# Kernel tuning notes

Hardware: AMD Instinct MI355X
Metric: run time of the kernel (lower is better)

## Reference

```python
import jax, jax.numpy as jnp
import numpy as np

NUM_TOKENS = 8192
D_MODEL = 512
D_FF = 1024
NUM_EXPERTS = 8
TOP_K = 2


def setup_inputs() -> dict:
    key = jax.random.key(0)
    k_x, k_r, k_w1, k_w2 = jax.random.split(key, 4)
    x = jax.random.normal(k_x, (NUM_TOKENS, D_MODEL), dtype=jnp.float32)
    # Router weight [num_experts, d_model]
    w_router = jax.random.normal(k_r, (NUM_EXPERTS, D_MODEL), dtype=jnp.float32) * 0.02
    # Expert weights stored as [E, N, K] (kernel convention: y = x @ W.T)
    w1 = jax.random.normal(k_w1, (NUM_EXPERTS, D_FF, D_MODEL), dtype=jnp.float32) * 0.02
    w2 = jax.random.normal(k_w2, (NUM_EXPERTS, D_MODEL, D_FF), dtype=jnp.float32) * 0.02
    return {"x": x, "w_router": w_router, "w1": w1, "w2": w2}


def reference(x, w_router, w1, w2):
    # Router: softmax over experts, top-k selection, renormalized gates
    logits = jnp.einsum("td,ed->te", x, w_router)            # [T, E]
    probs = jax.nn.softmax(logits, axis=-1)
    top_vals, top_idx = jax.lax.top_k(probs, TOP_K)           # [T, k]
    top_vals = top_vals / jnp.sum(top_vals, axis=-1, keepdims=True)

    # Combine weights per (token, expert): topk weight if selected else 0.
    # out[t] = sum_e gate[t,e] * W2[e] @ silu(W1[e] @ x[t])
    out = jnp.zeros_like(x)
    for e in range(NUM_EXPERTS):
        gate_e = jnp.sum(jnp.where(top_idx == e, top_vals, 0.0), axis=-1)  # [T]
        h = jax.nn.silu(jnp.einsum("td,fd->tf", x, w1[e]))                 # [T, d_ff]
        y = jnp.einsum("tf,df->td", h, w2[e])                              # [T, d]
        out = out + gate_e[:, None] * y
    return out
```

## Files before the change

### kernel.cpp

```cpp
#include <hip/hip_runtime.h>
#include <hip/hip_bf16.h>

#define NT 8192
#define DM 512
#define DF 1024
#define NE 8
#define MAXROWS (NT*2)

typedef __bf16 bf16_8 __attribute__((ext_vector_type(8)));
typedef float  f32_4  __attribute__((ext_vector_type(4)));
typedef unsigned short us8 __attribute__((ext_vector_type(8)));

__device__ inline unsigned short f2bf(float f) {
    unsigned int u = __float_as_uint(f);
    u = u + 0x7fffu + ((u >> 16) & 1u);
    return (unsigned short)(u >> 16);
}

__device__ inline bf16_8 as_bf(us8 v) { return __builtin_bit_cast(bf16_8, v); }

__device__ inline void gld16(const unsigned short* g, unsigned short* l) {
    __builtin_amdgcn_global_load_lds(
        (const __attribute__((address_space(1))) unsigned int*)g,
        (__attribute__((address_space(3))) unsigned int*)l, 16, 0, 0);
}

__global__ __launch_bounds__(256) void cast_kernel(const float* __restrict__ in,
                                                   unsigned short* __restrict__ out,
                                                   int n4) {
    int i = blockIdx.x * 256 + threadIdx.x;
    if (i >= n4) return;
    float4 v = ((const float4*)in)[i];
    ushort4 o;
    o.x = f2bf(v.x); o.y = f2bf(v.y); o.z = f2bf(v.z); o.w = f2bf(v.w);
    ((ushort4*)out)[i] = o;
}

__global__ __launch_bounds__(256) void router_kernel(const float* __restrict__ x,
                                                     const float* __restrict__ wr,
                                                     int* __restrict__ eidx,
                                                     float2* __restrict__ gates) {
    const int wid = threadIdx.x >> 6;
    const int lane = threadIdx.x & 63;
    const int t = blockIdx.x * 4 + wid;

    const float4* xrow = (const float4*)(x + (size_t)t * DM);
    float4 xv0 = xrow[lane * 2];
    float4 xv1 = xrow[lane * 2 + 1];

    float logit[NE];
#pragma unroll
    for (int e = 0; e < NE; ++e) {
        const float4* wrow = (const float4*)(wr + (size_t)e * DM);
        float4 w0 = wrow[lane * 2];
        float4 w1v = wrow[lane * 2 + 1];
        float s = xv0.x * w0.x + xv0.y * w0.y + xv0.z * w0.z + xv0.w * w0.w
                + xv1.x * w1v.x + xv1.y * w1v.y + xv1.z * w1v.z + xv1.w * w1v.w;
#pragma unroll
        for (int off = 32; off >= 1; off >>= 1) s += __shfl_xor(s, off);
        logit[e] = s;
    }

    if (lane == 0) {
        int i0 = 0; float m0 = logit[0];
#pragma unroll
        for (int e = 1; e < NE; ++e) if (logit[e] > m0) { m0 = logit[e]; i0 = e; }
        int i1 = -1; float m1 = -1e30f;
#pragma unroll
        for (int e = 0; e < NE; ++e) if (e != i0 && logit[e] > m1) { m1 = logit[e]; i1 = e; }
        float d = expf(m1 - m0);
        float g0 = 1.0f / (1.0f + d);
        float g1 = 1.0f - g0;
        eidx[t] = i0 | (i1 << 8);
        gates[t] = make_float2(g0, g1);
    }
}

__global__ __launch_bounds__(256) void build_lists_kernel(const int* __restrict__ eidx,
                                                          const float2* __restrict__ gates,
                                                          int* __restrict__ counts,
                                                          int* __restrict__ token_list,
                                                          float* __restrict__ gate_list) {
    const int e = blockIdx.x;
    const int tid = threadIdx.x;
    const int wid = tid >> 6, lane = tid & 63;
    __shared__ int wsum[4];
    __shared__ int base;
    if (tid == 0) base = 0;
    __syncthreads();
    for (int c = 0; c < NT; c += 256) {
        int t = c + tid;
        int ei = eidx[t];
        int i0 = ei & 0xff, i1 = (ei >> 8) & 0xff;
        bool match0 = (i0 == e), match1 = (i1 == e);
        bool m = match0 || match1;
        unsigned long long mask = __ballot(m);
        if (lane == 0) wsum[wid] = __popcll(mask);
        __syncthreads();
        int pre = 0;
#pragma unroll
        for (int w = 0; w < 4; ++w) if (w < wid) pre += wsum[w];
        int tot = wsum[0] + wsum[1] + wsum[2] + wsum[3];
        if (m) {
            int pos = base + pre + __popcll(mask & ((1ULL << lane) - 1ULL));
            token_list[e * NT + pos] = t;
            float2 g = gates[t];
            gate_list[e * NT + pos] = match0 ? g.x : g.y;
        }
        __syncthreads();
        if (tid == 0) base += tot;
        __syncthreads();
    }
    if (tid == 0) counts[e] = base;
}

__global__ void scan_kernel(const int* __restrict__ counts, int* __restrict__ offsets) {
    if (threadIdx.x == 0) {
        int s = 0;
        for (int e = 0; e < NE; ++e) { offsets[e] = s; s += counts[e]; }
    }
}

template <bool G1>
__global__ __launch_bounds__(256, 2) void moe_gemm(const unsigned short* __restrict__ Abase,
                                                   const unsigned short* __restrict__ Wbase,
                                                   unsigned short* __restrict__ h_out,
                                                   float* __restrict__ out,
                                                   const int* __restrict__ counts,
                                                   const int* __restrict__ offsets,
                                                   const int* __restrict__ token_list,
                                                   const float* __restrict__ gate_list) {
    constexpr int K = G1 ? DM : DF;
    constexpr int NCOLS = G1 ? DF : DM;
    constexpr int NSTEP = K / 64;
    constexpr int TILE_E = 128 * 64;
    const int e = blockIdx.z;
    const int cnt = counts[e];
    const int row0 = blockIdx.y * 128;
    if (row0 >= cnt) return;
    const int col0 = blockIdx.x * 128;
    const int off_e = offsets[e];

    __shared__ __align__(16) unsigned short Alds[2 * TILE_E];
    __shared__ __align__(16) unsigned short Blds[2 * TILE_E];

    const int tid = threadIdx.x;
    const int wid = tid >> 6;
    const int lane = tid & 63;

    const int g_oct = (lane & 7) ^ (lane >> 3);
    const unsigned short* gA[4];
    const unsigned short* gB[4];
    int ldsOff[4];
#pragma unroll
    for (int j = 0; j < 4; ++j) {
        int row_j = wid * 32 + j * 8 + (lane >> 3);
        int rr = min(row0 + row_j, cnt - 1);
        if (G1) {
            gA[j] = Abase + (size_t)token_list[e * NT + rr] * K + g_oct * 8;
        } else {
            gA[j] = Abase + (size_t)(off_e + rr) * K + g_oct * 8;
        }
        gB[j] = Wbase + ((size_t)e * NCOLS + col0 + row_j) * K + g_oct * 8;
        ldsOff[j] = (wid * 256 + j * 64) * 8;
    }

    const int wr = wid >> 1, wc = wid & 1;
    const int lrow = lane & 15;
    const int kc = lane >> 4;

    f32_4 acc[4][4];
#pragma unroll
    for (int m = 0; m < 4; ++m)
#pragma unroll
        for (int n = 0; n < 4; ++n) acc[m][n] = (f32_4){0.f, 0.f, 0.f, 0.f};

    auto issue = [&](int t) {
        int bb = t & 1;
        unsigned short* A_l = Alds + bb * TILE_E;
        unsigned short* B_l = Blds + bb * TILE_E;
        int k0 = t * 64;
#pragma unroll
        for (int j = 0; j < 4; ++j) {
            gld16(gA[j] + k0, A_l + ldsOff[j]);
            gld16(gB[j] + k0, B_l + ldsOff[j]);
        }
    };

    issue(0);
    for (int t = 0; t < NSTEP; ++t) {
        if (t + 1 < NSTEP) {
            issue(t + 1);
            asm volatile("s_waitcnt vmcnt(8)" ::: "memory");
        } else {
            asm volatile("s_waitcnt vmcnt(0)" ::: "memory");
        }
        __builtin_amdgcn_sched_barrier(0);
        __builtin_amdgcn_s_barrier();

        const unsigned short* A_l = Alds + (t & 1) * TILE_E;
        const unsigned short* B_l = Blds + (t & 1) * TILE_E;
#pragma unroll
        for (int s = 0; s < 2; ++s) {
            bf16_8 a[4], b[4];
#pragma unroll
            for (int m = 0; m < 4; ++m) {
                int row = wr * 64 + m * 16 + lrow;
                int oct = (s * 4 + kc) ^ (lrow & 7);
                a[m] = as_bf(*(const us8*)(A_l + row * 64 + oct * 8));
            }
#pragma unroll
            for (int n = 0; n < 4; ++n) {
                int row = wc * 64 + n * 16 + lrow;
                int oct = (s * 4 + kc) ^ (lrow & 7);
                b[n] = as_bf(*(const us8*)(B_l + row * 64 + oct * 8));
            }
#pragma unroll
            for (int m = 0; m < 4; ++m)
#pragma unroll
                for (int n = 0; n < 4; ++n)
                    acc[m][n] = __builtin_amdgcn_mfma_f32_16x16x32_bf16(a[m], b[n], acc[m][n], 0, 0, 0);
        }

        asm volatile("s_waitcnt lgkmcnt(0)" ::: "memory");
        __builtin_amdgcn_sched_barrier(0);
        __builtin_amdgcn_s_barrier();
    }

#pragma unroll
    for (int m = 0; m < 4; ++m) {
#pragma unroll
        for (int n = 0; n < 4; ++n) {
#pragma unroll
            for (int q = 0; q < 4; ++q) {
                int lr = wr * 64 + m * 16 + (lane >> 4) * 4 + q;
                int lc = wc * 64 + n * 16 + (lane & 15);
                int r = row0 + lr;
                if (r < cnt) {
                    float v = acc[m][n][q];
                    if (G1) {
                        v = v / (1.0f + expf(-v));
                        h_out[(size_t)(off_e + r) * DF + col0 + lc] = f2bf(v);
                    } else {
                        float g = gate_list[e * NT + r];
                        int tok = token_list[e * NT + r];
                        atomicAdd(&out[(size_t)tok * DM + col0 + lc], g * v);
                    }
                }
            }
        }
    }
}

extern "C" void kernel_launch(void* const* d_in, const int* in_sizes, int n_in,
                              void* d_out, int out_size, void* d_ws, size_t ws_size,
                              hipStream_t stream) {
    const float* x   = (const float*)d_in[0];
    const float* wrt = (const float*)d_in[1];
    const float* w1  = (const float*)d_in[2];
    const float* w2  = (const float*)d_in[3];
    float* out = (float*)d_out;

    char* ws = (char*)d_ws;
    size_t o = 0;
    auto alloc = [&](size_t bytes) { size_t r = o; o += (bytes + 255) & ~255UL; return r; };
    unsigned short* x_bf  = (unsigned short*)(ws + alloc((size_t)NT * DM * 2));
    unsigned short* w1_bf = (unsigned short*)(ws + alloc((size_t)NE * DF * DM * 2));
    unsigned short* w2_bf = (unsigned short*)(ws + alloc((size_t)NE * DM * DF * 2));
    unsigned short* h_bf  = (unsigned short*)(ws + alloc((size_t)MAXROWS * DF * 2));
    int*   counts     = (int*)(ws + alloc(NE * 4));
    int*   offsets    = (int*)(ws + alloc(NE * 4));
    int*   token_list = (int*)(ws + alloc((size_t)NE * NT * 4));
    float* gate_list  = (float*)(ws + alloc((size_t)NE * NT * 4));
    int*   eidx       = (int*)(ws + alloc((size_t)NT * 4));
    float2* gates     = (float2*)(ws + alloc((size_t)NT * 8));

    hipMemsetAsync(out, 0, (size_t)NT * DM * 4, stream);

    int n4x = NT * DM / 4;
    cast_kernel<<<(n4x + 255) / 256, 256, 0, stream>>>(x, x_bf, n4x);
    int n4w = NE * DF * DM / 4;
    cast_kernel<<<(n4w + 255) / 256, 256, 0, stream>>>(w1, w1_bf, n4w);
    cast_kernel<<<(n4w + 255) / 256, 256, 0, stream>>>(w2, w2_bf, n4w);

    router_kernel<<<NT / 4, 256, 0, stream>>>(x, wrt, eidx, gates);
    build_lists_kernel<<<NE, 256, 0, stream>>>(eidx, gates, counts, token_list, gate_list);
    scan_kernel<<<1, 64, 0, stream>>>(counts, offsets);

    moe_gemm<true><<<dim3(DF / 128, NT / 128, NE), 256, 0, stream>>>(
        x_bf, w1_bf, h_bf, nullptr, counts, offsets, token_list, gate_list);
    moe_gemm<false><<<dim3(DM / 128, NT / 128, NE), 256, 0, stream>>>(
        h_bf, w2_bf, nullptr, out, counts, offsets, token_list, gate_list);
}
```

Measured before the change: 190.0 us.

## Enlarge MoE GEMM tiles to 256 rows with 512-thread blocks

Grows the expert GEMM block tile from 128x128 to 256x256 for the first GEMM and 256x128 for the second, using 8 waves per block and 8xNF MFMA accumulators per wave. The global-to-LDS load mapping is reorganised to match, and the vmcnt wait counts are set per GEMM. The larger tiles raise arithmetic intensity and reuse of each loaded A and B tile, cutting global and LDS traffic per FLOP. In exchange it needs more registers and LDS per block, which may lower occupancy, and it wastes more padding rows on experts whose token count is not a multiple of 256.

```diff
diff --git a/kernel.cpp b/kernel.cpp
--- a/kernel.cpp
+++ b/kernel.cpp
@@ -122,7 +122,7 @@
 }
 
 template <bool G1>
-__global__ __launch_bounds__(256, 2) void moe_gemm(const unsigned short* __restrict__ Abase,
+__global__ __launch_bounds__(512, 2) void moe_gemm(const unsigned short* __restrict__ Abase,
                                                    const unsigned short* __restrict__ Wbase,
                                                    unsigned short* __restrict__ h_out,
                                                    float* __restrict__ out,
@@ -132,93 +132,106 @@
                                                    const float* __restrict__ gate_list) {
     constexpr int K = G1 ? DM : DF;
     constexpr int NCOLS = G1 ? DF : DM;
+    constexpr int BN = G1 ? 256 : 128;
+    constexpr int NF = BN / 64;
     constexpr int NSTEP = K / 64;
-    constexpr int TILE_E = 128 * 64;
+    constexpr int TA = 256 * 64;
+    constexpr int TB = BN * 64;
+
     const int e = blockIdx.z;
     const int cnt = counts[e];
-    const int row0 = blockIdx.y * 128;
+    const int row0 = blockIdx.y * 256;
     if (row0 >= cnt) return;
-    const int col0 = blockIdx.x * 128;
+    const int col0 = blockIdx.x * BN;
     const int off_e = offsets[e];
 
-    __shared__ __align__(16) unsigned short Alds[2 * TILE_E];
-    __shared__ __align__(16) unsigned short Blds[2 * TILE_E];
+    __shared__ __align__(16) unsigned short Alds[2 * TA];
+    __shared__ __align__(16) unsigned short Blds[2 * TB];
 
     const int tid = threadIdx.x;
     const int wid = tid >> 6;
     const int lane = tid & 63;
 
-    const int g_oct = (lane & 7) ^ (lane >> 3);
+    const int s_row = tid >> 3;
+    const int g_oct = (tid & 7) ^ (s_row & 7);
     const unsigned short* gA[4];
-    const unsigned short* gB[4];
-    int ldsOff[4];
+    int ldsA[4];
 #pragma unroll
     for (int j = 0; j < 4; ++j) {
-        int row_j = wid * 32 + j * 8 + (lane >> 3);
+        int row_j = j * 64 + s_row;
         int rr = min(row0 + row_j, cnt - 1);
         if (G1) {
             gA[j] = Abase + (size_t)token_list[e * NT + rr] * K + g_oct * 8;
         } else {
             gA[j] = Abase + (size_t)(off_e + rr) * K + g_oct * 8;
         }
+        ldsA[j] = (j * 512 + wid * 64) * 8;
+    }
+    const unsigned short* gB[NF];
+    int ldsB[NF];
+#pragma unroll
+    for (int j = 0; j < NF; ++j) {
+        int row_j = j * 64 + s_row;
         gB[j] = Wbase + ((size_t)e * NCOLS + col0 + row_j) * K + g_oct * 8;
-        ldsOff[j] = (wid * 256 + j * 64) * 8;
-    }
-
-    const int wr = wid >> 1, wc = wid & 1;
+        ldsB[j] = (j * 512 + wid * 64) * 8;
+    }
+
+    const int wr = wid >> 2, wc = wid & 3;
     const int lrow = lane & 15;
     const int kc = lane >> 4;
 
-    f32_4 acc[4][4];
-#pragma unroll
-    for (int m = 0; m < 4; ++m)
-#pragma unroll
-        for (int n = 0; n < 4; ++n) acc[m][n] = (f32_4){0.f, 0.f, 0.f, 0.f};
+    f32_4 acc[8][NF];
+#pragma unroll
+    for (int m = 0; m < 8; ++m)
+#pragma unroll
+        for (int n = 0; n < NF; ++n) acc[m][n] = (f32_4){0.f, 0.f, 0.f, 0.f};
 
     auto issue = [&](int t) {
         int bb = t & 1;
-        unsigned short* A_l = Alds + bb * TILE_E;
-        unsigned short* B_l = Blds + bb * TILE_E;
+        unsigned short* A_l = Alds + bb * TA;
+        unsigned short* B_l = Blds + bb * TB;
         int k0 = t * 64;
 #pragma unroll
-        for (int j = 0; j < 4; ++j) {
-            gld16(gA[j] + k0, A_l + ldsOff[j]);
-            gld16(gB[j] + k0, B_l + ldsOff[j]);
-        }
+        for (int j = 0; j < 4; ++j) gld16(gA[j] + k0, A_l + ldsA[j]);
+#pragma unroll
+        for (int j = 0; j < NF; ++j) gld16(gB[j] + k0, B_l + ldsB[j]);
     };
 
     issue(0);
     for (int t = 0; t < NSTEP; ++t) {
         if (t + 1 < NSTEP) {
             issue(t + 1);
-            asm volatile("s_waitcnt vmcnt(8)" ::: "memory");
+            if (G1) {
+                asm volatile("s_waitcnt vmcnt(8)" ::: "memory");
+            } else {
+                asm volatile("s_waitcnt vmcnt(6)" ::: "memory");
+            }
         } else {
             asm volatile("s_waitcnt vmcnt(0)" ::: "memory");
         }
         __builtin_amdgcn_sched_barrier(0);
         __builtin_amdgcn_s_barrier();
 
-        const unsigned short* A_l = Alds + (t & 1) * TILE_E;
-        const unsigned short* B_l = Blds + (t & 1) * TILE_E;
-#pragma unroll
-        for (int s = 0; s < 2; ++s) {
-            bf16_8 a[4], b[4];
-#pragma unroll
-            for (int m = 0; m < 4; ++m) {
-                int row = wr * 64 + m * 16 + lrow;
-                int oct = (s * 4 + kc) ^ (lrow & 7);
+        const unsigned short* A_l = Alds + (t & 1) * TA;
+        const unsigned short* B_l = Blds + (t & 1) * TB;
+#pragma unroll
+        for (int kh = 0; kh < 2; ++kh) {
+            bf16_8 a[8], b[NF];
+            const int oct = (kh * 4 + kc) ^ (lrow & 7);
+#pragma unroll
+            for (int m = 0; m < 8; ++m) {
+                int row = wr * 128 + m * 16 + lrow;
                 a[m] = as_bf(*(const us8*)(A_l + row * 64 + oct * 8));
             }
 #pragma unroll
-            for (int n = 0; n < 4; ++n) {
-                int row = wc * 64 + n * 16 + lrow;
-                int oct = (s * 4 + kc) ^ (lrow & 7);
+            for (int n = 0; n < NF; ++n) {
+                int row = wc * (NF * 16) + n * 16 + lrow;
                 b[n] = as_bf(*(const us8*)(B_l + row * 64 + oct * 8));
             }
 #pragma unroll
-            for (int m = 0; m < 4; ++m)
-#pragma unroll
-                for (int n = 0; n < 4; ++n)
+            for (int m = 0; m < 8; ++m)
+#pragma unroll
+                for (int n = 0; n < NF; ++n)
                     acc[m][n] = __builtin_amdgcn_mfma_f32_16x16x32_bf16(a[m], b[n], acc[m][n], 0, 0, 0);
         }
 
@@ -228,13 +241,13 @@
     }
 
 #pragma unroll
-    for (int m = 0; m < 4; ++m) {
-#pragma unroll
-        for (int n = 0; n < 4; ++n) {
+    for (int m = 0; m < 8; ++m) {
+#pragma unroll
+        for (int n = 0; n < NF; ++n) {
 #pragma unroll
             for (int q = 0; q < 4; ++q) {
-                int lr = wr * 64 + m * 16 + (lane >> 4) * 4 + q;
-                int lc = wc * 64 + n * 16 + (lane & 15);
+                int lr = wr * 128 + m * 16 + (lane >> 4) * 4 + q;
+                int lc = wc * (NF * 16) + n * 16 + (lane & 15);
                 int r = row0 + lr;
                 if (r < cnt) {
                     float v = acc[m][n][q];
@@ -287,8 +300,8 @@
     build_lists_kernel<<<NE, 256, 0, stream>>>(eidx, gates, counts, token_list, gate_list);
     scan_kernel<<<1, 64, 0, stream>>>(counts, offsets);
 
-    moe_gemm<true><<<dim3(DF / 128, NT / 128, NE), 256, 0, stream>>>(
+    moe_gemm<true><<<dim3(DF / 256, NT / 256, NE), 512, 0, stream>>>(
         x_bf, w1_bf, h_bf, nullptr, counts, offsets, token_list, gate_list);
-    moe_gemm<false><<<dim3(DM / 128, NT / 128, NE), 256, 0, stream>>>(
+    moe_gemm<false><<<dim3(DM / 128, NT / 256, NE), 512, 0, stream>>>(
         h_bf, w2_bf, nullptr, out, counts, offsets, token_list, gate_list);
 }
```

Result: slower. 212.2 us (+11.7%).
